# Kernel tuning notes

Measured on AMD Instinct MI355X. Metric: run time of the kernel, lower is better.

The kernel has to match this reference:

```python
import jax, jax.numpy as jnp
import numpy as np

B, CIN, REL, OUT, SH, H, W = 8, 256, 16, 64, 8, 56, 56
HW = H * W
K = 7          # window size
DIL = 2        # dilation
EPS = 1e-5


def conv1x1(x, w, b=None):
    # x: [B,C,h,w], w: [O,C]
    y = jnp.einsum('oc,bchw->bohw', w, x)
    if b is not None:
        y = y + b[None, :, None, None]
    return y


def bn_eval(x, g, b, m, v):
    scale = g / jnp.sqrt(v + EPS)
    return x * scale[None, :, None, None] + (b - m * scale)[None, :, None, None]


def unfold49(x, pad_reflect, pad_zero):
    # x: [B,C,H,W] -> [B,C,49,H,W]; 7x7 window, dilation 2, stride 1.
    if pad_reflect:
        x = jnp.pad(x, ((0, 0), (0, 0), (pad_reflect, pad_reflect), (pad_reflect, pad_reflect)), mode='reflect')
    if pad_zero:
        x = jnp.pad(x, ((0, 0), (0, 0), (pad_zero, pad_zero), (pad_zero, pad_zero)))
    patches = [x[:, :, DIL * i:DIL * i + H, DIL * j:DIL * j + W]
               for i in range(K) for j in range(K)]
    return jnp.stack(patches, axis=2)


def setup_inputs() -> dict:
    key = jax.random.key(0)
    ks = jax.random.split(key, 12)
    s_in = 1.0 / np.sqrt(CIN)
    inp = {
        'x': jax.random.normal(ks[0], (B, CIN, H, W), jnp.float32),
        'w1': jax.random.normal(ks[1], (REL, CIN), jnp.float32) * s_in,
        'b1': jax.random.normal(ks[2], (REL,), jnp.float32) * 0.01,
        'w2': jax.random.normal(ks[3], (REL, CIN), jnp.float32) * s_in,
        'b2': jax.random.normal(ks[4], (REL,), jnp.float32) * 0.01,
        'w3': jax.random.normal(ks[5], (OUT, CIN), jnp.float32) * s_in,
        'b3': jax.random.normal(ks[6], (OUT,), jnp.float32) * 0.01,
        'bn1_g': jax.random.uniform(ks[7], (REL * (K * K + 1),), jnp.float32, 0.5, 1.5),
        'bn1_b': jax.random.normal(ks[8], (REL * (K * K + 1),), jnp.float32) * 0.01,
        'bn1_m': jnp.zeros((REL * (K * K + 1),), jnp.float32),
        'bn1_v': jnp.ones((REL * (K * K + 1),), jnp.float32),
        'wcw1': jax.random.normal(ks[9], (OUT // SH, REL * (K * K + 1)), jnp.float32) * (1.0 / np.sqrt(REL * 50)),
        'bn2_g': jax.random.uniform(ks[10], (OUT // SH,), jnp.float32, 0.5, 1.5),
        'bn2_b': jnp.zeros((OUT // SH,), jnp.float32),
        'bn2_m': jnp.zeros((OUT // SH,), jnp.float32),
        'bn2_v': jnp.ones((OUT // SH,), jnp.float32),
        'wcw2': jax.random.normal(ks[11], (K * K * OUT // SH, OUT // SH), jnp.float32) * (1.0 / np.sqrt(OUT // SH)),
        'bcw2': jnp.zeros((K * K * OUT // SH,), jnp.float32),
    }
    return inp


def reference(x, w1, b1, w2, b2, w3, b3, bn1_g, bn1_b, bn1_m, bn1_v,
              wcw1, bn2_g, bn2_b, bn2_m, bn2_v, wcw2, bcw2):
    x1 = conv1x1(x, w1, b1)                      # [B,REL,H,W]
    x2 = conv1x1(x, w2, b2)                      # [B,REL,H,W]
    x3 = conv1x1(x, w3, b3)                      # [B,OUT,H,W]

    # x1 -> [B,REL,1,HW]
    x1f = x1.reshape(B, REL, 1, HW)
    # x2: ReflectionPad2d(2) then Unfold(7, dilation=2, padding=4) -> [B,REL*49,1,HW]
    x2u = unfold49(x2, pad_reflect=2, pad_zero=4).reshape(B, REL * K * K, 1, HW)

    cat = jnp.concatenate([x1f, x2u], axis=1)    # [B, REL*50, 1, HW]
    t = jax.nn.relu(bn_eval(cat, bn1_g, bn1_b, bn1_m, bn1_v))
    t = conv1x1(t, wcw1)                         # [B, OUT/SH, 1, HW], no bias
    t = jax.nn.relu(bn_eval(t, bn2_g, bn2_b, bn2_m, bn2_v))
    wmap = conv1x1(t, wcw2, bcw2)                # [B, 49*OUT/SH, 1, HW]
    wmap = wmap.reshape(B, OUT // SH, K * K, HW)  # channel layout wc*49+k

    # Aggregation(7, 1, 6, 2, pad_mode=1): reflect-pad 6, 7x7 dilated unfold,
    # out[b,c,n] = sum_k unf[b,c,k,n] * w[b, c//SH, k, n]
    x3u = unfold49(x3, pad_reflect=6, pad_zero=0).reshape(B, OUT // SH, SH, K * K, HW)
    out = jnp.einsum('bgskn,bgkn->bgsn', x3u, wmap).reshape(B, OUT, H, W)
    return out
```

## Files before the change

kernel.cpp:

```cpp
#include <hip/hip_runtime.h>
#include <hip/hip_bf16.h>

#define HW    3136
#define HH    56
#define NCIN  256
#define KK    49
#define PH    68
#define PP    (PH*PH)

#define OFF_WT    0
#define OFF_BCAT  24576
#define OFF_TAB   24672
#define OFF_WTAB  34272
#define OFF_B2F   38976
#define OFF_X1    39040
#define OFF_X2P   440448
#define OFF_X3P   1032320

__global__ __launch_bounds__(256) void kprep(
    const float* __restrict__ w1, const float* __restrict__ b1,
    const float* __restrict__ w2, const float* __restrict__ b2,
    const float* __restrict__ w3, const float* __restrict__ b3,
    const float* __restrict__ bn1g, const float* __restrict__ bn1b,
    const float* __restrict__ bn1m, const float* __restrict__ bn1v,
    const float* __restrict__ wcw1,
    const float* __restrict__ bn2g, const float* __restrict__ bn2b,
    const float* __restrict__ bn2m, const float* __restrict__ bn2v,
    const float* __restrict__ wcw2, const float* __restrict__ bcw2,
    float* __restrict__ ws)
{
    int idx = blockIdx.x * 256 + threadIdx.x;
    if (idx < 24576) {
        int o = idx >> 8, c = idx & 255;
        float v = (o < 16) ? w1[o * 256 + c]
                : (o < 32) ? w2[(o - 16) * 256 + c]
                           : w3[(o - 32) * 256 + c];
        ws[OFF_WT + c * 96 + o] = v;
    }
    int i2 = idx - 24576;
    if (i2 >= 0 && i2 < 96) {
        float v = (i2 < 16) ? b1[i2] : (i2 < 32) ? b2[i2 - 16] : b3[i2 - 32];
        ws[OFF_BCAT + i2] = v;
    }
    int i3 = idx - 24672;
    if (i3 >= 0 && i3 < 9600) {
        int row = i3 / 12, c = i3 - row * 12;
        int uu = row >> 4, r = row & 15;
        int j = (uu < 49) ? (16 + r * KK + uu) : r;
        float val = 0.f;
        if (c == 0) {
            val = bn1g[j] / sqrtf(bn1v[j] + 1e-5f);
        } else if (c == 1) {
            float s = bn1g[j] / sqrtf(bn1v[j] + 1e-5f);
            val = bn1b[j] - bn1m[j] * s;
        } else if (c < 10) {
            int e = c - 2;
            float s2 = bn2g[e] / sqrtf(bn2v[e] + 1e-5f);
            val = wcw1[e * 800 + j] * s2;
        }
        ws[OFF_TAB + i3] = val;
    }
    int i4 = idx - 34272;
    if (i4 >= 0 && i4 < 4704) {
        int row = i4 / 12, c = i4 - row * 12;
        float val = 0.f;
        if (c == 0)      val = bcw2[row];
        else if (c < 9)  val = wcw2[row * 8 + (c - 1)];
        ws[OFF_WTAB + i4] = val;
    }
    int i5 = idx - 38976;
    if (i5 >= 0 && i5 < 8) {
        float s2 = bn2g[i5] / sqrtf(bn2v[i5] + 1e-5f);
        ws[OFF_B2F + i5] = bn2b[i5] - bn2m[i5] * s2;
    }
}

__global__ __launch_bounds__(512) void kconv(
    const float* __restrict__ x, const float* __restrict__ wT,
    const float* __restrict__ bcat, float* __restrict__ x1out,
    float* __restrict__ x2pad, float* __restrict__ x3pad)
{
    __shared__ float xl[64][64];
    const int tid = threadIdx.x;
    const int l   = tid & 63;
    const int wv  = __builtin_amdgcn_readfirstlane(tid >> 6);
    const int b   = blockIdx.x / 49;
    const int bi  = blockIdx.x % 49;
    const int hw0 = bi * 64;
    const int ob  = wv * 12;

    if (bi < 8) {
        int z = bi * 512 + tid;
        int quad = z >> 10, cell = z & 1023;
        int p, q;
        if (cell < 272)      { p = cell / 68;  q = cell - p * 68; }
        else if (cell < 544) { int c2 = cell - 272; int pr = c2 / 68; p = 64 + pr; q = c2 - pr * 68; }
        else                 { int c2 = cell - 544; p = 4 + (c2 >> 3); int qq = c2 & 7; q = (qq < 4) ? qq : 60 + qq; }
        *(float4*)(x2pad + (((size_t)b * 4 + quad) * PP + p * PH + q) * 4) =
            make_float4(0.f, 0.f, 0.f, 0.f);
    }

    float acc[12];
    const float* bc = bcat + ob;
#pragma unroll
    for (int i = 0; i < 12; ++i) acc[i] = bc[i];

    const float* xb = x + (size_t)b * NCIN * HW + hw0;

    for (int cc = 0; cc < 4; ++cc) {
        __syncthreads();
#pragma unroll
        for (int i = 0; i < 8; ++i)
            xl[i * 8 + wv][l] = xb[(size_t)(cc * 64 + i * 8 + wv) * HW + l];
        __syncthreads();

        const float* wp = wT + (cc * 64) * 96 + ob;
#pragma unroll 4
        for (int k = 0; k < 64; ++k) {
            float xv = xl[k][l];
            const float4* wq = (const float4*)(wp + k * 96);
            float4 A = wq[0], B = wq[1], C = wq[2];
            acc[0]  = fmaf(xv, A.x, acc[0]);  acc[1]  = fmaf(xv, A.y, acc[1]);
            acc[2]  = fmaf(xv, A.z, acc[2]);  acc[3]  = fmaf(xv, A.w, acc[3]);
            acc[4]  = fmaf(xv, B.x, acc[4]);  acc[5]  = fmaf(xv, B.y, acc[5]);
            acc[6]  = fmaf(xv, B.z, acc[6]);  acc[7]  = fmaf(xv, B.w, acc[7]);
            acc[8]  = fmaf(xv, C.x, acc[8]);  acc[9]  = fmaf(xv, C.y, acc[9]);
            acc[10] = fmaf(xv, C.z, acc[10]); acc[11] = fmaf(xv, C.w, acc[11]);
        }
    }

    const int n  = hw0 + l;
    const int y  = n / HH;
    const int xx = n - y * HH;
    const int p0 = y + 6, q0 = xx + 6;
    const int yr3 = (y >= 1 && y <= 6) ? 6 - y : ((y >= 49 && y <= 54) ? 116 - y : -1);
    const int xr3 = (xx >= 1 && xx <= 6) ? 6 - xx : ((xx >= 49 && xx <= 54) ? 116 - xx : -1);
    const int yr2 = (y == 1 || y == 2) ? 6 - y : ((y == 53 || y == 54) ? 116 - y : -1);
    const int xr2 = (xx == 1 || xx == 2) ? 6 - xx : ((xx == 53 || xx == 54) ? 116 - xx : -1);
    const int cell0 = p0 * PH + q0;

#pragma unroll
    for (int qg = 0; qg < 3; ++qg) {
        const int ch0 = ob + qg * 4;
        float4 v = make_float4(acc[qg * 4], acc[qg * 4 + 1],
                               acc[qg * 4 + 2], acc[qg * 4 + 3]);
        if (ch0 < 16) {
            *(float4*)(x1out + (((size_t)b * 4 + (ch0 >> 2)) * HW + n) * 4) = v;
        } else if (ch0 < 32) {
            float* base = x2pad + ((size_t)b * 4 + ((ch0 - 16) >> 2)) * PP * 4;
            *(float4*)(base + (size_t)cell0 * 4) = v;
            if (yr2 >= 0)             *(float4*)(base + (size_t)(yr2 * PH + q0) * 4)  = v;
            if (xr2 >= 0)             *(float4*)(base + (size_t)(p0 * PH + xr2) * 4)  = v;
            if (yr2 >= 0 && xr2 >= 0) *(float4*)(base + (size_t)(yr2 * PH + xr2) * 4) = v;
        } else {
            float* base = x3pad + ((size_t)b * 16 + ((ch0 - 32) >> 2)) * PP * 4;
            *(float4*)(base + (size_t)cell0 * 4) = v;
            if (yr3 >= 0)             *(float4*)(base + (size_t)(yr3 * PH + q0) * 4)  = v;
            if (xr3 >= 0)             *(float4*)(base + (size_t)(p0 * PH + xr3) * 4)  = v;
            if (yr3 >= 0 && xr3 >= 0) *(float4*)(base + (size_t)(yr3 * PH + xr3) * 4) = v;
        }
    }
}

__global__ __launch_bounds__(512) void kmainB(
    const float* __restrict__ x1, const float* __restrict__ x2pad,
    const float* __restrict__ x3pad, const float* __restrict__ tab,
    const float* __restrict__ b2f, const float* __restrict__ wtab,
    float* __restrict__ out)
{
    __shared__ float red[8][8][64];
    __shared__ float tl[8][64];
    const int tid = threadIdx.x;
    const int w   = __builtin_amdgcn_readfirstlane(tid >> 6);
    const int l   = tid & 63;
    const int b   = blockIdx.x / 49;
    const int nb  = (blockIdx.x % 49) * 64;
    const int n   = nb + l;
    const int y   = n / HH;
    const int xx  = n - y * HH;

    float acc[8];
#pragma unroll
    for (int g = 0; g < 8; ++g) acc[g] = 0.f;

    const int u0 = (50 * w) >> 3;
    const int u1 = (50 * (w + 1)) >> 3;

#pragma unroll 2
    for (int u = u0; u < u1; ++u) {
        const float* trow;
        const float* xp;
        size_t qstr;
        if (u == 0) {
            trow = tab + 49 * 192;
            xp   = x1 + ((size_t)b * 4 * HW + n) * 4;
            qstr = (size_t)HW * 4;
        } else {
            const int kk = u - 1;
            const int i  = kk / 7;
            const int jj = kk - i * 7;
            trow = tab + kk * 192;
            xp   = x2pad + ((size_t)b * 4 * PP + (y + 2 * i) * PH + (xx + 2 * jj)) * 4;
            qstr = (size_t)PP * 4;
        }
        float vr[16];
        *(float4*)&vr[0]  = *(const float4*)xp;
        *(float4*)&vr[4]  = *(const float4*)(xp + qstr);
        *(float4*)&vr[8]  = *(const float4*)(xp + 2 * qstr);
        *(float4*)&vr[12] = *(const float4*)(xp + 3 * qstr);
#pragma unroll
        for (int r = 0; r < 16; ++r) {
            const float4* tq = (const float4*)(trow + r * 12);
            float4 A = tq[0], Bv = tq[1], Cv = tq[2];
            float v = fmaxf(fmaf(vr[r], A.x, A.y), 0.f);
            acc[0] = fmaf(v, A.z, acc[0]);  acc[1] = fmaf(v, A.w, acc[1]);
            acc[2] = fmaf(v, Bv.x, acc[2]); acc[3] = fmaf(v, Bv.y, acc[3]);
            acc[4] = fmaf(v, Bv.z, acc[4]); acc[5] = fmaf(v, Bv.w, acc[5]);
            acc[6] = fmaf(v, Cv.x, acc[6]); acc[7] = fmaf(v, Cv.y, acc[7]);
        }
    }

#pragma unroll
    for (int g = 0; g < 8; ++g) red[w][g][l] = acc[g];
    __syncthreads();

    {
        const int g  = tid >> 6;
        const int px = tid & 63;
        float s = b2f[g];
#pragma unroll
        for (int ww = 0; ww < 8; ++ww) s += red[ww][g][px];
        tl[g][px] = fmaxf(s, 0.f);
    }
    __syncthreads();

    const int g = w;
    float t[8];
#pragma unroll
    for (int e = 0; e < 8; ++e) t[e] = tl[e][l];

    float a2[8];
#pragma unroll
    for (int s = 0; s < 8; ++s) a2[s] = 0.f;

    const float* x3b = x3pad + ((size_t)(b * 16 + g * 2) * PP) * 4;
    const float* wg  = wtab + (size_t)g * KK * 12;

#pragma unroll 2
    for (int i = 0; i < 7; ++i) {
        const int rowc = (y + 2 * i) * PH + xx;
#pragma unroll
        for (int jj = 0; jj < 7; ++jj) {
            const int k = i * 7 + jj;
            const float* wrow = wg + k * 12;
            const float4* wq = (const float4*)wrow;
            float4 A = wq[0], Bv = wq[1];
            float w7 = wrow[8];
            float wv = A.x;
            wv = fmaf(t[0], A.y, wv);  wv = fmaf(t[1], A.z, wv);
            wv = fmaf(t[2], A.w, wv);  wv = fmaf(t[3], Bv.x, wv);
            wv = fmaf(t[4], Bv.y, wv); wv = fmaf(t[5], Bv.z, wv);
            wv = fmaf(t[6], Bv.w, wv); wv = fmaf(t[7], w7, wv);

            const float* xp = x3b + (size_t)(rowc + 2 * jj) * 4;
            float4 s0 = *(const float4*)xp;
            float4 s1 = *(const float4*)(xp + (size_t)PP * 4);
            a2[0] = fmaf(s0.x, wv, a2[0]); a2[1] = fmaf(s0.y, wv, a2[1]);
            a2[2] = fmaf(s0.z, wv, a2[2]); a2[3] = fmaf(s0.w, wv, a2[3]);
            a2[4] = fmaf(s1.x, wv, a2[4]); a2[5] = fmaf(s1.y, wv, a2[5]);
            a2[6] = fmaf(s1.z, wv, a2[6]); a2[7] = fmaf(s1.w, wv, a2[7]);
        }
    }

    float* op = out + ((size_t)b * 64 + g * 8) * HW + n;
#pragma unroll
    for (int s = 0; s < 8; ++s) op[(size_t)s * HW] = a2[s];
}

extern "C" void kernel_launch(void* const* d_in, const int* in_sizes, int n_in,
                              void* d_out, int out_size, void* d_ws, size_t ws_size,
                              hipStream_t stream) {
    const float* x    = (const float*)d_in[0];
    const float* w1   = (const float*)d_in[1];
    const float* b1   = (const float*)d_in[2];
    const float* w2   = (const float*)d_in[3];
    const float* b2   = (const float*)d_in[4];
    const float* w3   = (const float*)d_in[5];
    const float* b3   = (const float*)d_in[6];
    const float* bn1g = (const float*)d_in[7];
    const float* bn1b = (const float*)d_in[8];
    const float* bn1m = (const float*)d_in[9];
    const float* bn1v = (const float*)d_in[10];
    const float* wcw1 = (const float*)d_in[11];
    const float* bn2g = (const float*)d_in[12];
    const float* bn2b = (const float*)d_in[13];
    const float* bn2m = (const float*)d_in[14];
    const float* bn2v = (const float*)d_in[15];
    const float* wcw2 = (const float*)d_in[16];
    const float* bcw2 = (const float*)d_in[17];

    float* ws = (float*)d_ws;

    kprep<<<153, 256, 0, stream>>>(w1, b1, w2, b2, w3, b3,
                                   bn1g, bn1b, bn1m, bn1v, wcw1,
                                   bn2g, bn2b, bn2m, bn2v, wcw2, bcw2, ws);
    kconv<<<392, 512, 0, stream>>>(x, ws + OFF_WT, ws + OFF_BCAT,
                                   ws + OFF_X1, ws + OFF_X2P, ws + OFF_X3P);
    kmainB<<<392, 512, 0, stream>>>(ws + OFF_X1, ws + OFF_X2P, ws + OFF_X3P,
                                    ws + OFF_TAB, ws + OFF_B2F, ws + OFF_WTAB,
                                    (float*)d_out);
}
```

Before: 74.18 us.

## Split fused main kernel into t-computation and aggregation kernels with 1024 threads

Splits the fused kernel into two launches. The first computes the 8-channel t vector per pixel using 16 waves, each reducing a slice of the 50 unfold positions, and writes t to a workspace buffer. The second recomputes the weight map per pixel and aggregates with 16 waves per block, each covering half of a group's 4 channels. This doubles wave-level parallelism in both phases to hide memory latency better. It costs an extra launch, a global round trip for t, and duplicated weight-map FMAs across the two half-group waves.

```diff
diff --git a/kernel.cpp b/kernel.cpp
--- a/kernel.cpp
+++ b/kernel.cpp
@@ -16,6 +16,7 @@
 #define OFF_X1    39040
 #define OFF_X2P   440448
 #define OFF_X3P   1032320
+#define OFF_TB    3399808
 
 __global__ __launch_bounds__(256) void kprep(
     const float* __restrict__ w1, const float* __restrict__ b1,
@@ -162,14 +163,12 @@
     }
 }
 
-__global__ __launch_bounds__(512) void kmainB(
+__global__ __launch_bounds__(1024) void kt(
     const float* __restrict__ x1, const float* __restrict__ x2pad,
-    const float* __restrict__ x3pad, const float* __restrict__ tab,
-    const float* __restrict__ b2f, const float* __restrict__ wtab,
-    float* __restrict__ out)
+    const float* __restrict__ tab, const float* __restrict__ b2f,
+    float* __restrict__ tbuf)
 {
-    __shared__ float red[8][8][64];
-    __shared__ float tl[8][64];
+    __shared__ float red[16][8][64];
     const int tid = threadIdx.x;
     const int w   = __builtin_amdgcn_readfirstlane(tid >> 6);
     const int l   = tid & 63;
@@ -183,8 +182,8 @@
 #pragma unroll
     for (int g = 0; g < 8; ++g) acc[g] = 0.f;
 
-    const int u0 = (50 * w) >> 3;
-    const int u1 = (50 * (w + 1)) >> 3;
+    const int u0 = (50 * w) >> 4;
+    const int u1 = (50 * (w + 1)) >> 4;
 
 #pragma unroll 2
     for (int u = u0; u < u1; ++u) {
@@ -224,26 +223,41 @@
     for (int g = 0; g < 8; ++g) red[w][g][l] = acc[g];
     __syncthreads();
 
-    {
+    if (tid < 512) {
         const int g  = tid >> 6;
         const int px = tid & 63;
         float s = b2f[g];
 #pragma unroll
-        for (int ww = 0; ww < 8; ++ww) s += red[ww][g][px];
-        tl[g][px] = fmaxf(s, 0.f);
-    }
-    __syncthreads();
-
-    const int g = w;
+        for (int sl = 0; sl < 16; ++sl) s += red[sl][g][px];
+        tbuf[((size_t)b * HW + nb + px) * 8 + g] = fmaxf(s, 0.f);
+    }
+}
+
+__global__ __launch_bounds__(1024) void kagg(
+    const float* __restrict__ x3pad, const float* __restrict__ tbuf,
+    const float* __restrict__ wtab, float* __restrict__ out)
+{
+    const int tid  = threadIdx.x;
+    const int wv16 = tid >> 6;
+    const int g    = __builtin_amdgcn_readfirstlane(wv16 >> 1);
+    const int sh   = __builtin_amdgcn_readfirstlane(wv16 & 1);
+    const int l    = tid & 63;
+    const int b    = blockIdx.x / 49;
+    const int nb   = (blockIdx.x % 49) * 64;
+    const int n    = nb + l;
+    const int y    = n / HH;
+    const int xx   = n - y * HH;
+
     float t[8];
-#pragma unroll
-    for (int e = 0; e < 8; ++e) t[e] = tl[e][l];
-
-    float a2[8];
-#pragma unroll
-    for (int s = 0; s < 8; ++s) a2[s] = 0.f;
-
-    const float* x3b = x3pad + ((size_t)(b * 16 + g * 2) * PP) * 4;
+    {
+        const float* tp = tbuf + ((size_t)b * HW + n) * 8;
+        *(float4*)&t[0] = *(const float4*)tp;
+        *(float4*)&t[4] = *(const float4*)(tp + 4);
+    }
+
+    float a2[4] = {0.f, 0.f, 0.f, 0.f};
+
+    const float* x3b = x3pad + ((size_t)(b * 16 + g * 2 + sh) * PP) * 4;
     const float* wg  = wtab + (size_t)g * KK * 12;
 
 #pragma unroll 2
@@ -256,25 +270,21 @@
             const float4* wq = (const float4*)wrow;
             float4 A = wq[0], Bv = wq[1];
             float w7 = wrow[8];
-            float wv = A.x;
-            wv = fmaf(t[0], A.y, wv);  wv = fmaf(t[1], A.z, wv);
-            wv = fmaf(t[2], A.w, wv);  wv = fmaf(t[3], Bv.x, wv);
-            wv = fmaf(t[4], Bv.y, wv); wv = fmaf(t[5], Bv.z, wv);
-            wv = fmaf(t[6], Bv.w, wv); wv = fmaf(t[7], w7, wv);
-
-            const float* xp = x3b + (size_t)(rowc + 2 * jj) * 4;
-            float4 s0 = *(const float4*)xp;
-            float4 s1 = *(const float4*)(xp + (size_t)PP * 4);
-            a2[0] = fmaf(s0.x, wv, a2[0]); a2[1] = fmaf(s0.y, wv, a2[1]);
-            a2[2] = fmaf(s0.z, wv, a2[2]); a2[3] = fmaf(s0.w, wv, a2[3]);
-            a2[4] = fmaf(s1.x, wv, a2[4]); a2[5] = fmaf(s1.y, wv, a2[5]);
-            a2[6] = fmaf(s1.z, wv, a2[6]); a2[7] = fmaf(s1.w, wv, a2[7]);
-        }
-    }
-
-    float* op = out + ((size_t)b * 64 + g * 8) * HW + n;
-#pragma unroll
-    for (int s = 0; s < 8; ++s) op[(size_t)s * HW] = a2[s];
+            float wvv = A.x;
+            wvv = fmaf(t[0], A.y, wvv);  wvv = fmaf(t[1], A.z, wvv);
+            wvv = fmaf(t[2], A.w, wvv);  wvv = fmaf(t[3], Bv.x, wvv);
+            wvv = fmaf(t[4], Bv.y, wvv); wvv = fmaf(t[5], Bv.z, wvv);
+            wvv = fmaf(t[6], Bv.w, wvv); wvv = fmaf(t[7], w7, wvv);
+
+            float4 s0 = *(const float4*)(x3b + (size_t)(rowc + 2 * jj) * 4);
+            a2[0] = fmaf(s0.x, wvv, a2[0]); a2[1] = fmaf(s0.y, wvv, a2[1]);
+            a2[2] = fmaf(s0.z, wvv, a2[2]); a2[3] = fmaf(s0.w, wvv, a2[3]);
+        }
+    }
+
+    float* op = out + ((size_t)b * 64 + g * 8 + sh * 4) * HW + n;
+#pragma unroll
+    for (int s = 0; s < 4; ++s) op[(size_t)s * HW] = a2[s];
 }
 
 extern "C" void kernel_launch(void* const* d_in, const int* in_sizes, int n_in,
@@ -306,7 +316,8 @@
                                    bn2g, bn2b, bn2m, bn2v, wcw2, bcw2, ws);
     kconv<<<392, 512, 0, stream>>>(x, ws + OFF_WT, ws + OFF_BCAT,
                                    ws + OFF_X1, ws + OFF_X2P, ws + OFF_X3P);
-    kmainB<<<392, 512, 0, stream>>>(ws + OFF_X1, ws + OFF_X2P, ws + OFF_X3P,
-                                    ws + OFF_TAB, ws + OFF_B2F, ws + OFF_WTAB,
-                                    (float*)d_out);
-}
+    kt<<<392, 1024, 0, stream>>>(ws + OFF_X1, ws + OFF_X2P,
+                                 ws + OFF_TAB, ws + OFF_B2F, ws + OFF_TB);
+    kagg<<<392, 1024, 0, stream>>>(ws + OFF_X3P, ws + OFF_TB,
+                                   ws + OFF_WTAB, (float*)d_out);
+}
```

Result: slower. 76.07 us (+2.5%).

## Split conv1x1 blocks by output half and load x directly into registers

Applied to the files above, without the earlier changes.

The 1x1-conv kernel now launches twice as many 256-thread blocks, each covering half of the 96 output channels for a 64-pixel tile. The LDS staging of x and its barriers are removed. Each lane instead loads 16 input-channel values straight from global memory into registers per step. This targets barrier stalls and adds parallelism, but each x element is now read by two blocks, roughly doubling global/L2 reads of x.

```diff
diff --git a/kernel.cpp b/kernel.cpp
--- a/kernel.cpp
+++ b/kernel.cpp
@@ -75,22 +75,23 @@
     }
 }
 
-__global__ __launch_bounds__(512) void kconv(
+__global__ __launch_bounds__(256) void kconv(
     const float* __restrict__ x, const float* __restrict__ wT,
     const float* __restrict__ bcat, float* __restrict__ x1out,
     float* __restrict__ x2pad, float* __restrict__ x3pad)
 {
-    __shared__ float xl[64][64];
-    const int tid = threadIdx.x;
-    const int l   = tid & 63;
-    const int wv  = __builtin_amdgcn_readfirstlane(tid >> 6);
-    const int b   = blockIdx.x / 49;
-    const int bi  = blockIdx.x % 49;
-    const int hw0 = bi * 64;
-    const int ob  = wv * 12;
-
-    if (bi < 8) {
-        int z = bi * 512 + tid;
+    const int tid  = threadIdx.x;
+    const int l    = tid & 63;
+    const int wv   = __builtin_amdgcn_readfirstlane(tid >> 6);
+    const int bi   = blockIdx.x;
+    const int b    = bi / 98;
+    const int r98  = bi - b * 98;
+    const int half = r98 & 1;
+    const int hw0  = (r98 >> 1) * 64;
+    const int ob   = half * 48 + wv * 12;
+
+    if (r98 < 16) {
+        int z = r98 * 256 + tid;
         int quad = z >> 10, cell = z & 1023;
         int p, q;
         if (cell < 272)      { p = cell / 68;  q = cell - p * 68; }
@@ -105,27 +106,25 @@
 #pragma unroll
     for (int i = 0; i < 12; ++i) acc[i] = bc[i];
 
-    const float* xb = x + (size_t)b * NCIN * HW + hw0;
-
-    for (int cc = 0; cc < 4; ++cc) {
-        __syncthreads();
-#pragma unroll
-        for (int i = 0; i < 8; ++i)
-            xl[i * 8 + wv][l] = xb[(size_t)(cc * 64 + i * 8 + wv) * HW + l];
-        __syncthreads();
-
-        const float* wp = wT + (cc * 64) * 96 + ob;
-#pragma unroll 4
-        for (int k = 0; k < 64; ++k) {
-            float xv = xl[k][l];
-            const float4* wq = (const float4*)(wp + k * 96);
+    const float* xb = x + (size_t)b * NCIN * HW + hw0 + l;
+    const float* wb = wT + ob;
+
+#pragma unroll 1
+    for (int kb = 0; kb < NCIN; kb += 16) {
+        float xv[16];
+#pragma unroll
+        for (int i = 0; i < 16; ++i)
+            xv[i] = xb[(size_t)(kb + i) * HW];
+#pragma unroll
+        for (int i = 0; i < 16; ++i) {
+            const float4* wq = (const float4*)(wb + (kb + i) * 96);
             float4 A = wq[0], B = wq[1], C = wq[2];
-            acc[0]  = fmaf(xv, A.x, acc[0]);  acc[1]  = fmaf(xv, A.y, acc[1]);
-            acc[2]  = fmaf(xv, A.z, acc[2]);  acc[3]  = fmaf(xv, A.w, acc[3]);
-            acc[4]  = fmaf(xv, B.x, acc[4]);  acc[5]  = fmaf(xv, B.y, acc[5]);
-            acc[6]  = fmaf(xv, B.z, acc[6]);  acc[7]  = fmaf(xv, B.w, acc[7]);
-            acc[8]  = fmaf(xv, C.x, acc[8]);  acc[9]  = fmaf(xv, C.y, acc[9]);
-            acc[10] = fmaf(xv, C.z, acc[10]); acc[11] = fmaf(xv, C.w, acc[11]);
+            acc[0]  = fmaf(xv[i], A.x, acc[0]);  acc[1]  = fmaf(xv[i], A.y, acc[1]);
+            acc[2]  = fmaf(xv[i], A.z, acc[2]);  acc[3]  = fmaf(xv[i], A.w, acc[3]);
+            acc[4]  = fmaf(xv[i], B.x, acc[4]);  acc[5]  = fmaf(xv[i], B.y, acc[5]);
+            acc[6]  = fmaf(xv[i], B.z, acc[6]);  acc[7]  = fmaf(xv[i], B.w, acc[7]);
+            acc[8]  = fmaf(xv[i], C.x, acc[8]);  acc[9]  = fmaf(xv[i], C.y, acc[9]);
+            acc[10] = fmaf(xv[i], C.z, acc[10]); acc[11] = fmaf(xv[i], C.w, acc[11]);
         }
     }
 
@@ -304,7 +303,7 @@
     kprep<<<153, 256, 0, stream>>>(w1, b1, w2, b2, w3, b3,
                                    bn1g, bn1b, bn1m, bn1v, wcw1,
                                    bn2g, bn2b, bn2m, bn2v, wcw2, bcw2, ws);
-    kconv<<<392, 512, 0, stream>>>(x, ws + OFF_WT, ws + OFF_BCAT,
+    kconv<<<784, 256, 0, stream>>>(x, ws + OFF_WT, ws + OFF_BCAT,
                                    ws + OFF_X1, ws + OFF_X2P, ws + OFF_X3P);
     kmainB<<<392, 512, 0, stream>>>(ws + OFF_X1, ws + OFF_X2P, ws + OFF_X3P,
                                     ws + OFF_TAB, ws + OFF_B2F, ws + OFF_WTAB,
```

Measured after the change: 81.71 us. 10.1% more time.
